# Performance work log

Hardware: AMD Instinct MI355X
Metric: run time of the kernel (lower is better)

## Reference

```python
import jax, jax.numpy as jnp
import numpy as np

NUM_GROUPS = 2
NUM_VARS = 320
TAU = 2.0  # self.temperature
B, L, CONV_DIM = 8, 4096, 512
CODEVECTOR_DIM = 256


def setup_inputs() -> dict:
    key = jax.random.key(0)
    k1, k2, k3, k4, k5 = jax.random.split(key, 5)
    hidden_states = jax.random.normal(k1, (B, L, CONV_DIM), dtype=jnp.float32)
    gumbel_u = jax.random.uniform(k2, (B * L * NUM_GROUPS, NUM_VARS), dtype=jnp.float32)
    w_proj = jax.random.normal(k3, (CONV_DIM, NUM_GROUPS * NUM_VARS), dtype=jnp.float32) * 0.02
    b_proj = jax.random.normal(k4, (NUM_GROUPS * NUM_VARS,), dtype=jnp.float32) * 0.02
    codevectors = jax.random.normal(k5, (1, NUM_GROUPS * NUM_VARS, CODEVECTOR_DIM // NUM_GROUPS), dtype=jnp.float32)
    return {"hidden_states": hidden_states, "gumbel_u": gumbel_u,
            "w_proj": w_proj, "b_proj": b_proj, "codevectors": codevectors}


def reference(hidden_states, gumbel_u, w_proj, b_proj, codevectors):
    b, l, _ = hidden_states.shape
    G, V = NUM_GROUPS, NUM_VARS
    d = codevectors.shape[-1]

    # weight projection: [B, L, C] @ [C, G*V] -> [B, L, G*V] -> [(B*L*G), V]
    logits = (jnp.einsum('blc,cv->blv', hidden_states, w_proj) + b_proj)
    logits = logits.reshape(b * l * G, V)

    # gumbel-softmax (hard=True, training path) with explicit uniform noise
    eps = 1e-10
    gumbel = -jnp.log(-jnp.log(gumbel_u + eps) + eps)
    y_soft = jax.nn.softmax((logits + gumbel) / TAU, axis=-1)          # [(B*L*G), V]
    idx = jnp.argmax(y_soft, axis=-1)
    y_hard = jax.nn.one_hot(idx, V, dtype=y_soft.dtype)
    # straight-through estimator: hard forward, soft backward
    codevector_probs = y_hard - jax.lax.stop_gradient(y_soft) + y_soft  # [(B*L*G), V]

    # perplexity from the (noise-free) soft distribution, mask=None -> mean over sequences
    soft_dist = jax.nn.softmax(logits.reshape(b * l, G, V), axis=-1)
    avg_probs = jnp.mean(soft_dist, axis=0)                             # [G, V]
    perplexity = jnp.sum(jnp.exp(-jnp.sum(avg_probs * jnp.log(avg_probs + 1e-7), axis=-1)))

    # weighted sum over codevectors per group, then concat groups:
    # probs [(B*L), G, V] x codevectors [G, V, d] -> [(B*L), G, d]
    probs = codevector_probs.reshape(b * l, G, V)
    cv = codevectors.reshape(G, V, d)
    out = jnp.einsum('ngv,gvd->ngd', probs, cv).reshape(b, l, G * d)
    return out, perplexity
```

## Files before the change

### kernel.cpp

```cpp
#include <hip/hip_runtime.h>
#include <math.h>

#define NROWS 32768
#define CDIM  512
#define G_    2
#define V_    320
#define NCOLS 640
#define DCODE 128
#define NSLOT 64
#define BMR   32

typedef short bf16x8 __attribute__((ext_vector_type(8)));
typedef float f32x4  __attribute__((ext_vector_type(4)));

__device__ __forceinline__ short f2bf(float f) {
    union { float f; unsigned u; } v; v.f = f;
    unsigned r = v.u + 0x7FFFu + ((v.u >> 16) & 1u);
    return (short)(r >> 16);
}
__device__ __forceinline__ void gl_lds16(const void* g, void* l) {
    __builtin_amdgcn_global_load_lds(
        (const __attribute__((address_space(1))) unsigned int*)g,
        (__attribute__((address_space(3))) unsigned int*)l, 16, 0, 0);
}

__global__ __launch_bounds__(256) void wprep(const float* __restrict__ w,
                                             short* __restrict__ wpk) {
    int gid = blockIdx.x * 256 + threadIdx.x;
    int l15 = gid & 15, kq = (gid >> 4) & 3;
    int rem = gid >> 6;
    int tt16 = rem % 20; rem /= 20;
    int ts = rem & 15, g = rem >> 4;
    int n  = g * V_ + tt16 * 16 + l15;
    int k0 = ts * 32 + kq * 8;
    bf16x8 o;
    #pragma unroll
    for (int e = 0; e < 8; ++e) o[e] = f2bf(w[(size_t)(k0 + e) * NCOLS + n]);
    *(bf16x8*)&wpk[(size_t)gid * 8] = o;
}

__global__ __launch_bounds__(256) void hprep(const float* __restrict__ hidden,
                                             short* __restrict__ hpk) {
    int gid = blockIdx.x * 256 + threadIdx.x;
    int lane = gid & 63;
    int mf   = (gid >> 6) & 1;
    int ts   = (gid >> 7) & 15;
    int rb   = gid >> 11;
    int row  = rb * BMR + mf * 16 + (lane & 15);
    int k0   = ts * 32 + (lane >> 4) * 8;
    const float* src = hidden + (size_t)row * CDIM + k0;
    float4 a = *(const float4*)src;
    float4 b = *(const float4*)(src + 4);
    bf16x8 o;
    o[0]=f2bf(a.x); o[1]=f2bf(a.y); o[2]=f2bf(a.z); o[3]=f2bf(a.w);
    o[4]=f2bf(b.x); o[5]=f2bf(b.y); o[6]=f2bf(b.z); o[7]=f2bf(b.w);
    *(bf16x8*)&hpk[(size_t)gid * 8] = o;
}

__global__ __launch_bounds__(256, 4) void gvq_gemm(
    const short* __restrict__ hpk,
    const float* __restrict__ gumbel_u,
    const short* __restrict__ wpk,
    const float* __restrict__ bias,
    const float* __restrict__ cv,
    float* __restrict__ out,
    float* __restrict__ gavg)
{
    __shared__ short Hs[16384];
    __shared__ float s_psum[4][BMR];
    __shared__ float s_bestv[4][BMR];
    __shared__ int   s_besti[4][BMR];

    const int t    = threadIdx.x;
    const int wave = t >> 6;
    const int lane = t & 63;
    const int l15  = lane & 15;
    const int kq   = lane >> 4;
    const int tb   = wave * 5;
    const int rb   = blockIdx.x;
    const int g    = blockIdx.y;
    const int m0   = rb * BMR;

    const short* wbase = wpk + ((size_t)(g * 16) * 20 + tb) * 512 + (size_t)lane * 8;

    {
        const short* hsrc = hpk + (size_t)rb * 16384;
        #pragma unroll
        for (int i = 0; i < 8; ++i) {
            const int off = (wave * 8 + i) * 512;
            gl_lds16(hsrc + off + lane * 8, &Hs[off]);
        }
    }

    f32x4 acc[5][2];
    #pragma unroll
    for (int nf = 0; nf < 5; ++nf)
        #pragma unroll
        for (int mf = 0; mf < 2; ++mf)
            #pragma unroll
            for (int r = 0; r < 4; ++r) acc[nf][mf][r] = 0.f;

    bf16x8 bw[5];
    #pragma unroll
    for (int nf = 0; nf < 5; ++nf) bw[nf] = *(const bf16x8*)(wbase + nf * 512);

    __syncthreads();

    #pragma unroll
    for (int ts = 0; ts < 16; ++ts) {
        bf16x8 bn[5];
        if (ts < 15) {
            const short* wn = wbase + (ts + 1) * 10240;
            #pragma unroll
            for (int nf = 0; nf < 5; ++nf) bn[nf] = *(const bf16x8*)(wn + nf * 512);
        }
        bf16x8 hf0 = *(const bf16x8*)&Hs[ts * 1024 + lane * 8];
        bf16x8 hf1 = *(const bf16x8*)&Hs[ts * 1024 + 512 + lane * 8];
        #pragma unroll
        for (int nf = 0; nf < 5; ++nf)
            acc[nf][0] = __builtin_amdgcn_mfma_f32_16x16x32_bf16(bw[nf], hf0, acc[nf][0], 0, 0, 0);
        #pragma unroll
        for (int nf = 0; nf < 5; ++nf)
            acc[nf][1] = __builtin_amdgcn_mfma_f32_16x16x32_bf16(bw[nf], hf1, acc[nf][1], 0, 0, 0);
        #pragma unroll
        for (int nf = 0; nf < 5; ++nf) bw[nf] = bn[nf];
    }

    float4 bv4[5], u4[2][5];
    #pragma unroll
    for (int nf = 0; nf < 5; ++nf)
        bv4[nf] = *(const float4*)&bias[g * V_ + (tb + nf) * 16 + kq * 4];
    #pragma unroll
    for (int mf = 0; mf < 2; ++mf) {
        const float* up = gumbel_u + ((size_t)(m0 + mf * 16 + l15) * G_ + g) * V_;
        #pragma unroll
        for (int nf = 0; nf < 5; ++nf)
            u4[mf][nf] = *(const float4*)&up[(tb + nf) * 16 + kq * 4];
    }

    #pragma unroll
    for (int mf = 0; mf < 2; ++mf) {
        float s = 0.f, best = -1e30f; int bi = 0;
        #pragma unroll
        for (int nf = 0; nf < 5; ++nf) {
            #pragma unroll
            for (int r = 0; r < 4; ++r) {
                float z = fminf(acc[nf][mf][r] + bv4[nf][r], 60.f);
                float e = __expf(z);
                acc[nf][mf][r] = e;
                s += e;
                float u = (r == 0) ? u4[mf][nf].x : (r == 1) ? u4[mf][nf].y
                        : (r == 2) ? u4[mf][nf].z : u4[mf][nf].w;
                float wv = -__logf(u + 1e-10f) + 1e-10f;
                float ratio = e * __builtin_amdgcn_rcpf(wv);
                const int vi = (tb + nf) * 16 + kq * 4 + r;
                if (ratio > best) { best = ratio; bi = vi; }
            }
        }
        #pragma unroll
        for (int o = 16; o <= 32; o <<= 1) {
            s += __shfl_xor(s, o);
            float ov = __shfl_xor(best, o);
            int   oi = __shfl_xor(bi, o);
            if (ov > best || (ov == best && oi < bi)) { best = ov; bi = oi; }
        }
        if (kq == 0) {
            s_psum[wave][mf * 16 + l15]  = s;
            s_bestv[wave][mf * 16 + l15] = best;
            s_besti[wave][mf * 16 + l15] = bi;
        }
    }
    __syncthreads();

    float inv[2];
    #pragma unroll
    for (int mf = 0; mf < 2; ++mf) {
        const int rl = mf * 16 + l15;
        inv[mf] = 1.f / (s_psum[0][rl] + s_psum[1][rl] +
                         s_psum[2][rl] + s_psum[3][rl]);
    }
    float cpl[5][4];
    #pragma unroll
    for (int nf = 0; nf < 5; ++nf)
        #pragma unroll
        for (int r = 0; r < 4; ++r) {
            float v = acc[nf][0][r] * inv[0] + acc[nf][1][r] * inv[1];
            #pragma unroll
            for (int o = 1; o <= 8; o <<= 1) v += __shfl_xor(v, o);
            cpl[nf][r] = v;
        }
    float* gslot = gavg + (size_t)(rb & (NSLOT - 1)) * NCOLS;
    if (l15 == 0) {
        #pragma unroll
        for (int nf = 0; nf < 5; ++nf)
            #pragma unroll
            for (int r = 0; r < 4; ++r)
                atomicAdd(&gslot[g * V_ + (tb + nf) * 16 + kq * 4 + r], cpl[nf][r]);
    }

    {
        const int r_  = t >> 3;
        const int seg = t & 7;
        float best = s_bestv[0][r_]; int bi = s_besti[0][r_];
        #pragma unroll
        for (int q = 1; q < 4; ++q) {
            float v = s_bestv[q][r_];
            if (v > best) { best = v; bi = s_besti[q][r_]; }
        }
        const float* src = cv + ((size_t)g * V_ + bi) * DCODE + seg * 16;
        float* dst = out + (size_t)(m0 + r_) * (G_ * DCODE) + g * DCODE + seg * 16;
        #pragma unroll
        for (int j = 0; j < 4; ++j)
            *(float4*)(dst + j * 4) = *(const float4*)(src + j * 4);
    }
}

__global__ __launch_bounds__(1024) void gvq_perp(const float* __restrict__ gavg,
                                                 float* __restrict__ out)
{
    __shared__ float sp[NCOLS];
    const int t = threadIdx.x;
    if (t < NCOLS) {
        float a = 0.f;
        #pragma unroll
        for (int sb = 0; sb < 8; ++sb) {
            float p[8];
            #pragma unroll
            for (int j = 0; j < 8; ++j)
                p[j] = gavg[(size_t)(sb * 8 + j) * NCOLS + t];
            #pragma unroll
            for (int j = 0; j < 8; ++j) a += p[j];
        }
        sp[t] = a;
    }
    __syncthreads();
    if (t < 64) {
        float s0 = 0.f, s1 = 0.f;
        #pragma unroll
        for (int j = 0; j < 5; ++j) {
            float p0 = sp[t + j * 64]      * (1.f / NROWS);
            float p1 = sp[V_ + t + j * 64] * (1.f / NROWS);
            s0 += p0 * __logf(p0 + 1e-7f);
            s1 += p1 * __logf(p1 + 1e-7f);
        }
        #pragma unroll
        for (int o = 1; o < 64; o <<= 1) {
            s0 += __shfl_xor(s0, o);
            s1 += __shfl_xor(s1, o);
        }
        if (t == 0)
            out[(size_t)NROWS * (G_ * DCODE)] = expf(-s0) + expf(-s1);
    }
}

extern "C" void kernel_launch(void* const* d_in, const int* in_sizes, int n_in,
                              void* d_out, int out_size, void* d_ws, size_t ws_size,
                              hipStream_t stream)
{
    const float* hidden = (const float*)d_in[0];
    const float* gu     = (const float*)d_in[1];
    const float* w      = (const float*)d_in[2];
    const float* b      = (const float*)d_in[3];
    const float* cv     = (const float*)d_in[4];
    float* out  = (float*)d_out;
    float* gavg = (float*)d_ws;
    short* wpk  = (short*)((char*)d_ws + 163840);
    short* hpk  = (short*)((char*)d_ws + 819200);

    hipMemsetAsync(d_ws, 0, NSLOT * NCOLS * sizeof(float), stream);
    wprep<<<160, 256, 0, stream>>>(w, wpk);
    hprep<<<8192, 256, 0, stream>>>(hidden, hpk);
    gvq_gemm<<<dim3(NROWS / BMR, G_), 256, 0, stream>>>(hpk, gu, wpk, b, cv, out, gavg);
    gvq_perp<<<1, 1024, 0, stream>>>(gavg, out);
}
```

Measured before the change: 97.19 us.

## Make GEMM blocks persistent with register-resident weights and double-buffered LDS

The fused GEMM kernel becomes persistent: 256 blocks each keep their group's full weight slice in registers (80 bf16x8 per thread) and loop over 8 row-blocks. Hidden-state tiles are double-buffered in LDS, with the next tile prefetched while the current one is computed. The goal is to stop re-reading the weights from global memory in every block and to overlap tile loads with compute. In exchange, occupancy drops to about one block per CU because of register pressure, and only 256 blocks are launched, so latency hiding may be worse.

```diff
diff --git a/kernel.cpp b/kernel.cpp
--- a/kernel.cpp
+++ b/kernel.cpp
@@ -57,7 +57,7 @@
     *(bf16x8*)&hpk[(size_t)gid * 8] = o;
 }
 
-__global__ __launch_bounds__(256, 4) void gvq_gemm(
+__global__ __launch_bounds__(256, 1) void gvq_gemm(
     const short* __restrict__ hpk,
     const float* __restrict__ gumbel_u,
     const short* __restrict__ wpk,
@@ -66,7 +66,7 @@
     float* __restrict__ out,
     float* __restrict__ gavg)
 {
-    __shared__ short Hs[16384];
+    __shared__ short Hs[2][16384];
     __shared__ float s_psum[4][BMR];
     __shared__ float s_bestv[4][BMR];
     __shared__ int   s_besti[4][BMR];
@@ -77,141 +77,141 @@
     const int l15  = lane & 15;
     const int kq   = lane >> 4;
     const int tb   = wave * 5;
-    const int rb   = blockIdx.x;
-    const int g    = blockIdx.y;
-    const int m0   = rb * BMR;
+    const int b    = blockIdx.x;
+    const int g    = b & 1;
+    const int rb0  = (b >> 1) * 8;
 
     const short* wbase = wpk + ((size_t)(g * 16) * 20 + tb) * 512 + (size_t)lane * 8;
-
-    {
-        const short* hsrc = hpk + (size_t)rb * 16384;
-        #pragma unroll
-        for (int i = 0; i < 8; ++i) {
-            const int off = (wave * 8 + i) * 512;
-            gl_lds16(hsrc + off + lane * 8, &Hs[off]);
-        }
-    }
-
-    f32x4 acc[5][2];
+    bf16x8 warr[16][5];
     #pragma unroll
-    for (int nf = 0; nf < 5; ++nf)
-        #pragma unroll
-        for (int mf = 0; mf < 2; ++mf)
-            #pragma unroll
-            for (int r = 0; r < 4; ++r) acc[nf][mf][r] = 0.f;
-
-    bf16x8 bw[5];
-    #pragma unroll
-    for (int nf = 0; nf < 5; ++nf) bw[nf] = *(const bf16x8*)(wbase + nf * 512);
-
-    __syncthreads();
-
-    #pragma unroll
-    for (int ts = 0; ts < 16; ++ts) {
-        bf16x8 bn[5];
-        if (ts < 15) {
-            const short* wn = wbase + (ts + 1) * 10240;
-            #pragma unroll
-            for (int nf = 0; nf < 5; ++nf) bn[nf] = *(const bf16x8*)(wn + nf * 512);
-        }
-        bf16x8 hf0 = *(const bf16x8*)&Hs[ts * 1024 + lane * 8];
-        bf16x8 hf1 = *(const bf16x8*)&Hs[ts * 1024 + 512 + lane * 8];
+    for (int ts = 0; ts < 16; ++ts)
         #pragma unroll
         for (int nf = 0; nf < 5; ++nf)
-            acc[nf][0] = __builtin_amdgcn_mfma_f32_16x16x32_bf16(bw[nf], hf0, acc[nf][0], 0, 0, 0);
-        #pragma unroll
-        for (int nf = 0; nf < 5; ++nf)
-            acc[nf][1] = __builtin_amdgcn_mfma_f32_16x16x32_bf16(bw[nf], hf1, acc[nf][1], 0, 0, 0);
-        #pragma unroll
-        for (int nf = 0; nf < 5; ++nf) bw[nf] = bn[nf];
-    }
-
-    float4 bv4[5], u4[2][5];
+            warr[ts][nf] = *(const bf16x8*)(wbase + ts * 10240 + nf * 512);
+
+    float4 bv4[5];
     #pragma unroll
     for (int nf = 0; nf < 5; ++nf)
         bv4[nf] = *(const float4*)&bias[g * V_ + (tb + nf) * 16 + kq * 4];
-    #pragma unroll
-    for (int mf = 0; mf < 2; ++mf) {
-        const float* up = gumbel_u + ((size_t)(m0 + mf * 16 + l15) * G_ + g) * V_;
+
+    {
+        const short* hsrc = hpk + (size_t)rb0 * 16384;
+        #pragma unroll
+        for (int i = 0; i < 8; ++i) {
+            const int off = (wave * 8 + i) * 512;
+            gl_lds16(hsrc + off + lane * 8, &Hs[0][off]);
+        }
+    }
+
+    for (int task = 0; task < 8; ++task) {
+        const int rb  = rb0 + task;
+        const int cur = task & 1;
+        const int m0  = rb * BMR;
+
+        __syncthreads();
+
+        if (task < 7) {
+            const short* hsrc = hpk + (size_t)(rb + 1) * 16384;
+            #pragma unroll
+            for (int i = 0; i < 8; ++i) {
+                const int off = (wave * 8 + i) * 512;
+                gl_lds16(hsrc + off + lane * 8, &Hs[cur ^ 1][off]);
+            }
+        }
+
+        f32x4 acc[5][2];
         #pragma unroll
         for (int nf = 0; nf < 5; ++nf)
-            u4[mf][nf] = *(const float4*)&up[(tb + nf) * 16 + kq * 4];
-    }
-
-    #pragma unroll
-    for (int mf = 0; mf < 2; ++mf) {
-        float s = 0.f, best = -1e30f; int bi = 0;
-        #pragma unroll
-        for (int nf = 0; nf < 5; ++nf) {
+            #pragma unroll
+            for (int mf = 0; mf < 2; ++mf)
+                #pragma unroll
+                for (int r = 0; r < 4; ++r) acc[nf][mf][r] = 0.f;
+
+        #pragma unroll
+        for (int ts = 0; ts < 16; ++ts) {
+            bf16x8 hf0 = *(const bf16x8*)&Hs[cur][ts * 1024 + lane * 8];
+            bf16x8 hf1 = *(const bf16x8*)&Hs[cur][ts * 1024 + 512 + lane * 8];
+            #pragma unroll
+            for (int nf = 0; nf < 5; ++nf)
+                acc[nf][0] = __builtin_amdgcn_mfma_f32_16x16x32_bf16(warr[ts][nf], hf0, acc[nf][0], 0, 0, 0);
+            #pragma unroll
+            for (int nf = 0; nf < 5; ++nf)
+                acc[nf][1] = __builtin_amdgcn_mfma_f32_16x16x32_bf16(warr[ts][nf], hf1, acc[nf][1], 0, 0, 0);
+        }
+
+        #pragma unroll
+        for (int mf = 0; mf < 2; ++mf) {
+            const float* up = gumbel_u + ((size_t)(m0 + mf * 16 + l15) * G_ + g) * V_;
+            float4 u4[5];
+            #pragma unroll
+            for (int nf = 0; nf < 5; ++nf)
+                u4[nf] = *(const float4*)&up[(tb + nf) * 16 + kq * 4];
+            float s = 0.f, best = -1e30f; int bi = 0;
+            #pragma unroll
+            for (int nf = 0; nf < 5; ++nf) {
+                #pragma unroll
+                for (int r = 0; r < 4; ++r) {
+                    float z = fminf(acc[nf][mf][r] + bv4[nf][r], 60.f);
+                    float e = __expf(z);
+                    acc[nf][mf][r] = e;
+                    s += e;
+                    float u = (r == 0) ? u4[nf].x : (r == 1) ? u4[nf].y
+                            : (r == 2) ? u4[nf].z : u4[nf].w;
+                    float wv = -__logf(u + 1e-10f) + 1e-10f;
+                    float ratio = e * __builtin_amdgcn_rcpf(wv);
+                    const int vi = (tb + nf) * 16 + kq * 4 + r;
+                    if (ratio > best) { best = ratio; bi = vi; }
+                }
+            }
+            #pragma unroll
+            for (int o = 16; o <= 32; o <<= 1) {
+                s += __shfl_xor(s, o);
+                float ov = __shfl_xor(best, o);
+                int   oi = __shfl_xor(bi, o);
+                if (ov > best || (ov == best && oi < bi)) { best = ov; bi = oi; }
+            }
+            if (kq == 0) {
+                s_psum[wave][mf * 16 + l15]  = s;
+                s_bestv[wave][mf * 16 + l15] = best;
+                s_besti[wave][mf * 16 + l15] = bi;
+            }
+        }
+        __syncthreads();
+
+        float inv[2];
+        #pragma unroll
+        for (int mf = 0; mf < 2; ++mf) {
+            const int rl = mf * 16 + l15;
+            inv[mf] = 1.f / (s_psum[0][rl] + s_psum[1][rl] +
+                             s_psum[2][rl] + s_psum[3][rl]);
+        }
+        #pragma unroll
+        for (int nf = 0; nf < 5; ++nf)
             #pragma unroll
             for (int r = 0; r < 4; ++r) {
-                float z = fminf(acc[nf][mf][r] + bv4[nf][r], 60.f);
-                float e = __expf(z);
-                acc[nf][mf][r] = e;
-                s += e;
-                float u = (r == 0) ? u4[mf][nf].x : (r == 1) ? u4[mf][nf].y
-                        : (r == 2) ? u4[mf][nf].z : u4[mf][nf].w;
-                float wv = -__logf(u + 1e-10f) + 1e-10f;
-                float ratio = e * __builtin_amdgcn_rcpf(wv);
-                const int vi = (tb + nf) * 16 + kq * 4 + r;
-                if (ratio > best) { best = ratio; bi = vi; }
-            }
-        }
-        #pragma unroll
-        for (int o = 16; o <= 32; o <<= 1) {
-            s += __shfl_xor(s, o);
-            float ov = __shfl_xor(best, o);
-            int   oi = __shfl_xor(bi, o);
-            if (ov > best || (ov == best && oi < bi)) { best = ov; bi = oi; }
-        }
-        if (kq == 0) {
-            s_psum[wave][mf * 16 + l15]  = s;
-            s_bestv[wave][mf * 16 + l15] = best;
-            s_besti[wave][mf * 16 + l15] = bi;
-        }
-    }
-    __syncthreads();
-
-    float inv[2];
-    #pragma unroll
-    for (int mf = 0; mf < 2; ++mf) {
-        const int rl = mf * 16 + l15;
-        inv[mf] = 1.f / (s_psum[0][rl] + s_psum[1][rl] +
-                         s_psum[2][rl] + s_psum[3][rl]);
-    }
-    float cpl[5][4];
-    #pragma unroll
-    for (int nf = 0; nf < 5; ++nf)
-        #pragma unroll
-        for (int r = 0; r < 4; ++r) {
-            float v = acc[nf][0][r] * inv[0] + acc[nf][1][r] * inv[1];
-            #pragma unroll
-            for (int o = 1; o <= 8; o <<= 1) v += __shfl_xor(v, o);
-            cpl[nf][r] = v;
-        }
-    float* gslot = gavg + (size_t)(rb & (NSLOT - 1)) * NCOLS;
-    if (l15 == 0) {
-        #pragma unroll
-        for (int nf = 0; nf < 5; ++nf)
-            #pragma unroll
-            for (int r = 0; r < 4; ++r)
-                atomicAdd(&gslot[g * V_ + (tb + nf) * 16 + kq * 4 + r], cpl[nf][r]);
-    }
-
-    {
-        const int r_  = t >> 3;
-        const int seg = t & 7;
-        float best = s_bestv[0][r_]; int bi = s_besti[0][r_];
-        #pragma unroll
-        for (int q = 1; q < 4; ++q) {
-            float v = s_bestv[q][r_];
-            if (v > best) { best = v; bi = s_besti[q][r_]; }
-        }
-        const float* src = cv + ((size_t)g * V_ + bi) * DCODE + seg * 16;
-        float* dst = out + (size_t)(m0 + r_) * (G_ * DCODE) + g * DCODE + seg * 16;
-        #pragma unroll
-        for (int j = 0; j < 4; ++j)
-            *(float4*)(dst + j * 4) = *(const float4*)(src + j * 4);
+                float v = acc[nf][0][r] * inv[0] + acc[nf][1][r] * inv[1];
+                #pragma unroll
+                for (int o = 1; o <= 8; o <<= 1) v += __shfl_xor(v, o);
+                if (l15 == 0)
+                    atomicAdd(&gavg[(size_t)(rb & (NSLOT - 1)) * NCOLS
+                                    + g * V_ + (tb + nf) * 16 + kq * 4 + r], v);
+            }
+
+        {
+            const int r_  = t >> 3;
+            const int seg = t & 7;
+            float best = s_bestv[0][r_]; int bi = s_besti[0][r_];
+            #pragma unroll
+            for (int q = 1; q < 4; ++q) {
+                float v = s_bestv[q][r_];
+                if (v > best) { best = v; bi = s_besti[q][r_]; }
+            }
+            const float* src = cv + ((size_t)g * V_ + bi) * DCODE + seg * 16;
+            float* dst = out + (size_t)(m0 + r_) * (G_ * DCODE) + g * DCODE + seg * 16;
+            #pragma unroll
+            for (int j = 0; j < 4; ++j)
+                *(float4*)(dst + j * 4) = *(const float4*)(src + j * 4);
+        }
     }
 }
 
@@ -270,6 +270,6 @@
     hipMemsetAsync(d_ws, 0, NSLOT * NCOLS * sizeof(float), stream);
     wprep<<<160, 256, 0, stream>>>(w, wpk);
     hprep<<<8192, 256, 0, stream>>>(hidden, hpk);
-    gvq_gemm<<<dim3(NROWS / BMR, G_), 256, 0, stream>>>(hpk, gu, wpk, b, cv, out, gavg);
+    gvq_gemm<<<256, 256, 0, stream>>>(hpk, gu, wpk, b, cv, out, gavg);
     gvq_perp<<<1, 1024, 0, stream>>>(gavg, out);
 }
```

After: 127.1 us. +30.8%, slower.
